# Performance work log

Measured on AMD Instinct MI355X. Metric: run time of the kernel, lower is better.

Reference implementation:

```python
import jax, jax.numpy as jnp
import numpy as np

HOP = 256
FRAMELEN = 512
FILTERLEN = 64
WD = FILTERLEN // 2          # weights_delay default
WMIN, WMAX = -65535.0, 65535.0
MU = 0.05                    # LMS step size (concrete iterate)
B = 2
NFRAMES = 4096
T = FRAMELEN + HOP * (NFRAMES - 1)


def _unfold(a, size, step):
    # torch.Tensor.unfold along last dim -> (..., n_frames, size)
    n = (a.shape[-1] - size) // step + 1
    idx = np.arange(n)[:, None] * step + np.arange(size)[None, :]
    return a[..., idx]


def setup_inputs() -> dict:
    key = jax.random.key(0)
    kd, kx = jax.random.split(key)
    d = jax.random.normal(kd, (B, T), dtype=jnp.float32)
    x = jax.random.normal(kx, (T,), dtype=jnp.float32)
    return {"d": d, "x": x}


def reference(d, x):
    d_f = _unfold(d, FRAMELEN, HOP)            # (B, F, framelen)
    x_f = _unfold(x, FRAMELEN, HOP)[None]      # (1, F, framelen)
    Bn, F, _ = d_f.shape
    S = (FRAMELEN - FILTERLEN) - WD            # sequential steps per frame
    w0 = jnp.zeros((Bn, F, FILTERLEN), d.dtype)

    def step(w, t):
        # x window [t : t+filterlen]  (i = WD + t in the torch loop)
        xi = jax.lax.dynamic_slice_in_dim(x_f, t, FILTERLEN, axis=2)  # (1,F,K)
        d_est = jnp.sum(w * xi, axis=-1)       # einsum('ijk,pjk->ij', w, xi)
        e = d_f[..., WD + t] - d_est
        w = jnp.clip(w + MU * e[..., None] * xi, WMIN, WMAX)
        return w, (d_est, e)

    _, (d_est_s, e_s) = jax.lax.scan(step, w0, jnp.arange(S))

    def assemble(y):
        # (S,B,F) -> (B,F, framelen-filterlen), first WD slots stay zero
        y = jnp.moveaxis(y, 0, -1)
        return jnp.pad(y, ((0, 0), (0, 0), (WD, 0)))

    d_est = assemble(d_est_s)
    e = assemble(e_s)
    tail = FRAMELEN - HOP

    def ola(y):
        # first frame in full, then non-overlapping tail of each later frame
        return jnp.concatenate(
            [y[:, 0, :], y[:, 1:, tail:].reshape(y.shape[0], -1)], axis=-1)

    return ola(d_est), ola(e)
```

## Files before the change

kernel.cpp:

```cpp
#include <hip/hip_runtime.h>

#define HOP     256
#define WD      32
#define NFRM    4096
#define TLEN    1048832
#define LROW    786688
#define XSTR    484
#define DSTR    420
#define XQn     121
#define DQn     105
#define XTOT    (2*XSTR + 16)
#define GTOT    (4*DSTR + 8)

__device__ __forceinline__ float red16(float v) {
    v += __int_as_float(__builtin_amdgcn_update_dpp(0, __float_as_int(v), 0xB1,  0xF, 0xF, true));
    v += __int_as_float(__builtin_amdgcn_update_dpp(0, __float_as_int(v), 0x4E,  0xF, 0xF, true));
    v += __int_as_float(__builtin_amdgcn_update_dpp(0, __float_as_int(v), 0x141, 0xF, 0xF, true));
    v += __int_as_float(__builtin_amdgcn_update_dpp(0, __float_as_int(v), 0x140, 0xF, 0xF, true));
    return v;
}

#define CL(v) __builtin_amdgcn_fmed3f((v), -65535.0f, 65535.0f)

#define STEP1(Xa,Xb,Xc,Xd, GV, IND) do {                          \
    float p = w0 * (Xa);                                          \
    p = fmaf(w1, (Xb), p);                                        \
    p = fmaf(w2, (Xc), p);                                        \
    p = fmaf(w3, (Xd), p);                                        \
    float s  = red16(p);                                          \
    so = fmaf((IND), s, so);                                      \
    float gm = fmaf(-0.05f, s, (GV));                             \
    w0 = CL(fmaf(gm, (Xa), w0));                                  \
    w1 = CL(fmaf(gm, (Xb), w1));                                  \
    w2 = CL(fmaf(gm, (Xc), w2));                                  \
    w3 = CL(fmaf(gm, (Xd), w3));                                  \
} while (0)

#define GROUP4(QA, QB, GQ, Ia, Ib, Ic, Id) do {                   \
    STEP1(QA.x,QA.y,QA.z,QA.w, GQ.x, Ia);                         \
    STEP1(QA.y,QA.z,QA.w,QB.x, GQ.y, Ib);                         \
    STEP1(QA.z,QA.w,QB.x,QB.y, GQ.z, Ic);                         \
    STEP1(QA.w,QB.x,QB.y,QB.z, GQ.w, Id);                         \
} while (0)

__global__ void __launch_bounds__(64, 2)
lms_kernel(const float* __restrict__ dmat, const float* __restrict__ xvec,
           float* __restrict__ out)
{
    __shared__ __align__(16) float lx[XTOT];
    __shared__ __align__(16) float lg[GTOT];

    const int tid = threadIdx.x;
    const int f0  = blockIdx.x * 2;

    for (int i = tid; i < 242 + 420; i += 64) {
        if (i < 242) {
            int fr = (i >= XQn) ? 1 : 0;
            int k  = i - fr * XQn;
            ((float4*)lx)[i] =
                *(const float4*)(xvec + (size_t)(f0 + fr) * HOP + 4 * k);
        } else {
            int j   = i - 242;
            int idx = j / DQn, k = j - idx * DQn;
            int b = idx >> 1, r = idx & 1;
            float4 v = *(const float4*)(dmat + (size_t)b * TLEN
                                        + (size_t)(f0 + r) * HOP + WD + 4 * k);
            float4 g2;
            g2.x = 0.05f * v.x; g2.y = 0.05f * v.y;
            g2.z = 0.05f * v.z; g2.w = 0.05f * v.w;
            ((float4*)lg)[j] = g2;
        }
    }
    __syncthreads();

    const int lane = tid & 63;
    const int row  = lane >> 4;
    const int col  = lane & 15;
    const int fl   = row >> 1;
    const int b    = row & 1;
    const int f    = f0 + fl;
    const bool early = (f == 0);
    const int ci   = b * 2 + fl;

    const float4* __restrict__ xq  = (const float4*)(lx + fl * XSTR + 4 * col);
    const float4* __restrict__ gq  = (const float4*)(lg + ci * DSTR);
    const float*  __restrict__ lgs = lg + ci * DSTR;

    float* od = out + (size_t)b * LROW + 32 + (size_t)192 * f;
    float* oe = od + 2 * (size_t)LROW;

    if (blockIdx.x == 0) {
        int pos = tid & 31;
        for (int r2 = tid >> 5; r2 < 4; r2 += 2)
            out[(size_t)r2 * LROW + pos] = 0.0f;
    }

    const float i0  = (col ==  0) ? 1.f : 0.f, i1  = (col ==  1) ? 1.f : 0.f;
    const float i2  = (col ==  2) ? 1.f : 0.f, i3  = (col ==  3) ? 1.f : 0.f;
    const float i4  = (col ==  4) ? 1.f : 0.f, i5  = (col ==  5) ? 1.f : 0.f;
    const float i6  = (col ==  6) ? 1.f : 0.f, i7  = (col ==  7) ? 1.f : 0.f;
    const float i8  = (col ==  8) ? 1.f : 0.f, i9  = (col ==  9) ? 1.f : 0.f;
    const float i10 = (col == 10) ? 1.f : 0.f, i11 = (col == 11) ? 1.f : 0.f;
    const float i12 = (col == 12) ? 1.f : 0.f, i13 = (col == 13) ? 1.f : 0.f;
    const float i14 = (col == 14) ? 1.f : 0.f, i15 = (col == 15) ? 1.f : 0.f;

    float w0 = 0.f, w1 = 0.f, w2 = 0.f, w3 = 0.f;

    float4 X0 = xq[0], X1 = xq[1], X2 = xq[2];
    float4 G0 = gq[0], G1 = gq[1];

    for (int j = 0; j < 26; ++j) {
        const int g = 4 * j;
        float so  = 0.f;
        float gvs = lgs[16 * j + col];

        float4 X3 = xq[g+3];  float4 G2 = gq[g+2];
        GROUP4(X0, X1, G0, i0,  i1,  i2,  i3);

        X0 = xq[g+4];         float4 G3 = gq[g+3];
        GROUP4(X1, X2, G1, i4,  i5,  i6,  i7);

        X1 = xq[g+5];         G0 = gq[g+4];
        GROUP4(X2, X3, G2, i8,  i9,  i10, i11);

        X2 = xq[g+6];         G1 = gq[g+5];
        GROUP4(X3, X0, G3, i12, i13, i14, i15);

        if (j >= 14 || early) {
            float gms = fmaf(-0.05f, so, gvs);
            od[16 * j + col] = so;
            oe[16 * j + col] = 20.0f * gms;
        }
    }
}

extern "C" void kernel_launch(void* const* d_in, const int* in_sizes, int n_in,
                              void* d_out, int out_size, void* d_ws, size_t ws_size,
                              hipStream_t stream) {
    const float* dmat = (const float*)d_in[0];
    const float* xvec = (const float*)d_in[1];
    float* out = (float*)d_out;

    hipLaunchKernelGGL(lms_kernel, dim3(NFRM / 2), dim3(64), 0, stream,
                       dmat, xvec, out);
}
```

Baseline: 36.93 us.

## Interleave two independent LMS chains per lane to hide DPP reduction latency

Each wave now handles four frames instead of two, and each lane advances two independent frame recurrences (A and B) in lockstep. This interleaves their dot-product, DPP reduction and weight-update chains so one chain's latency can overlap the other's. The dot product is also split into two partial sums to shorten the dependency depth. The trade-off is half as many blocks (1024), more registers and LDS per block, and launch bounds lowered to one block per SIMD, which reduces wave-level parallelism across the GPU.

```diff
diff --git a/kernel.cpp b/kernel.cpp
--- a/kernel.cpp
+++ b/kernel.cpp
@@ -9,41 +9,47 @@
 #define DSTR    420
 #define XQn     121
 #define DQn     105
-#define XTOT    (2*XSTR + 16)
-#define GTOT    (4*DSTR + 8)
+#define XTOT    (4*XSTR + 16)
+#define GTOT    (8*DSTR + 8)
 
-__device__ __forceinline__ float red16(float v) {
-    v += __int_as_float(__builtin_amdgcn_update_dpp(0, __float_as_int(v), 0xB1,  0xF, 0xF, true));
-    v += __int_as_float(__builtin_amdgcn_update_dpp(0, __float_as_int(v), 0x4E,  0xF, 0xF, true));
-    v += __int_as_float(__builtin_amdgcn_update_dpp(0, __float_as_int(v), 0x141, 0xF, 0xF, true));
-    v += __int_as_float(__builtin_amdgcn_update_dpp(0, __float_as_int(v), 0x140, 0xF, 0xF, true));
-    return v;
+template<int C>
+__device__ __forceinline__ float dpa(float v) {
+    return v + __int_as_float(
+        __builtin_amdgcn_update_dpp(0, __float_as_int(v), C, 0xF, 0xF, true));
 }
 
 #define CL(v) __builtin_amdgcn_fmed3f((v), -65535.0f, 65535.0f)
 
-#define STEP1(Xa,Xb,Xc,Xd, GV, IND) do {                          \
-    float p = w0 * (Xa);                                          \
-    p = fmaf(w1, (Xb), p);                                        \
-    p = fmaf(w2, (Xc), p);                                        \
-    p = fmaf(w3, (Xd), p);                                        \
-    float s  = red16(p);                                          \
-    so = fmaf((IND), s, so);                                      \
-    float gm = fmaf(-0.05f, s, (GV));                             \
-    w0 = CL(fmaf(gm, (Xa), w0));                                  \
-    w1 = CL(fmaf(gm, (Xb), w1));                                  \
-    w2 = CL(fmaf(gm, (Xc), w2));                                  \
-    w3 = CL(fmaf(gm, (Xd), w3));                                  \
+#define STEP2(AXa,AXb,AXc,AXd,AGV, BXa,BXb,BXc,BXd,BGV, IND) do {        \
+    float ap0 = aw0 * (AXa);             float bp0 = bw0 * (BXa);        \
+    float ap1 = aw2 * (AXc);             float bp1 = bw2 * (BXc);        \
+    ap0 = fmaf(aw1, (AXb), ap0);         bp0 = fmaf(bw1, (BXb), bp0);    \
+    ap1 = fmaf(aw3, (AXd), ap1);         bp1 = fmaf(bw3, (BXd), bp1);    \
+    float ap = ap0 + ap1;                float bp = bp0 + bp1;           \
+    ap = dpa<0xB1>(ap);                  bp = dpa<0xB1>(bp);             \
+    ap = dpa<0x4E>(ap);                  bp = dpa<0x4E>(bp);             \
+    ap = dpa<0x141>(ap);                 bp = dpa<0x141>(bp);            \
+    ap = dpa<0x140>(ap);                 bp = dpa<0x140>(bp);            \
+    aso = fmaf((IND), ap, aso);          bso = fmaf((IND), bp, bso);     \
+    float agm = fmaf(-0.05f, ap, (AGV)); float bgm = fmaf(-0.05f, bp, (BGV)); \
+    aw0 = CL(fmaf(agm, (AXa), aw0));     bw0 = CL(fmaf(bgm, (BXa), bw0)); \
+    aw1 = CL(fmaf(agm, (AXb), aw1));     bw1 = CL(fmaf(bgm, (BXb), bw1)); \
+    aw2 = CL(fmaf(agm, (AXc), aw2));     bw2 = CL(fmaf(bgm, (BXc), bw2)); \
+    aw3 = CL(fmaf(agm, (AXd), aw3));     bw3 = CL(fmaf(bgm, (BXd), bw3)); \
 } while (0)
 
-#define GROUP4(QA, QB, GQ, Ia, Ib, Ic, Id) do {                   \
-    STEP1(QA.x,QA.y,QA.z,QA.w, GQ.x, Ia);                         \
-    STEP1(QA.y,QA.z,QA.w,QB.x, GQ.y, Ib);                         \
-    STEP1(QA.z,QA.w,QB.x,QB.y, GQ.z, Ic);                         \
-    STEP1(QA.w,QB.x,QB.y,QB.z, GQ.w, Id);                         \
+#define GROUP2(AQA,AQB,AGQ, BQA,BQB,BGQ, Ia,Ib,Ic,Id) do {               \
+    STEP2(AQA.x,AQA.y,AQA.z,AQA.w, AGQ.x,                                \
+          BQA.x,BQA.y,BQA.z,BQA.w, BGQ.x, Ia);                           \
+    STEP2(AQA.y,AQA.z,AQA.w,AQB.x, AGQ.y,                                \
+          BQA.y,BQA.z,BQA.w,BQB.x, BGQ.y, Ib);                           \
+    STEP2(AQA.z,AQA.w,AQB.x,AQB.y, AGQ.z,                                \
+          BQA.z,BQA.w,BQB.x,BQB.y, BGQ.z, Ic);                           \
+    STEP2(AQA.w,AQB.x,AQB.y,AQB.z, AGQ.w,                                \
+          BQA.w,BQB.x,BQB.y,BQB.z, BGQ.w, Id);                           \
 } while (0)
 
-__global__ void __launch_bounds__(64, 2)
+__global__ void __launch_bounds__(64, 1)
 lms_kernel(const float* __restrict__ dmat, const float* __restrict__ xvec,
            float* __restrict__ out)
 {
@@ -51,18 +57,17 @@
     __shared__ __align__(16) float lg[GTOT];
 
     const int tid = threadIdx.x;
-    const int f0  = blockIdx.x * 2;
+    const int f0  = blockIdx.x * 4;
 
-    for (int i = tid; i < 242 + 420; i += 64) {
-        if (i < 242) {
-            int fr = (i >= XQn) ? 1 : 0;
-            int k  = i - fr * XQn;
+    for (int i = tid; i < 484 + 840; i += 64) {
+        if (i < 484) {
+            int fr = i / XQn, k = i - fr * XQn;
             ((float4*)lx)[i] =
                 *(const float4*)(xvec + (size_t)(f0 + fr) * HOP + 4 * k);
         } else {
-            int j   = i - 242;
+            int j   = i - 484;
             int idx = j / DQn, k = j - idx * DQn;
-            int b = idx >> 1, r = idx & 1;
+            int b = idx >> 2, r = idx & 3;
             float4 v = *(const float4*)(dmat + (size_t)b * TLEN
                                         + (size_t)(f0 + r) * HOP + WD + 4 * k);
             float4 g2;
@@ -73,26 +78,31 @@
     }
     __syncthreads();
 
-    const int lane = tid & 63;
-    const int row  = lane >> 4;
-    const int col  = lane & 15;
-    const int fl   = row >> 1;
+    const int row  = tid >> 4;
+    const int col  = tid & 15;
+    const int flA  = row >> 1;
     const int b    = row & 1;
-    const int f    = f0 + fl;
-    const bool early = (f == 0);
-    const int ci   = b * 2 + fl;
+    const int fA   = f0 + flA;
+    const int fB   = fA + 2;
+    const bool earlyA = (fA == 0);
+    const int ciA  = b * 4 + flA;
+    const int ciB  = ciA + 2;
 
-    const float4* __restrict__ xq  = (const float4*)(lx + fl * XSTR + 4 * col);
-    const float4* __restrict__ gq  = (const float4*)(lg + ci * DSTR);
-    const float*  __restrict__ lgs = lg + ci * DSTR;
+    const float4* __restrict__ xqA = (const float4*)(lx + flA * XSTR + 4 * col);
+    const float4* __restrict__ xqB = (const float4*)(lx + (flA + 2) * XSTR + 4 * col);
+    const float4* __restrict__ gqA = (const float4*)(lg + ciA * DSTR);
+    const float4* __restrict__ gqB = (const float4*)(lg + ciB * DSTR);
+    const float*  __restrict__ lgsA = lg + ciA * DSTR;
+    const float*  __restrict__ lgsB = lg + ciB * DSTR;
 
-    float* od = out + (size_t)b * LROW + 32 + (size_t)192 * f;
-    float* oe = od + 2 * (size_t)LROW;
+    float* odA = out + (size_t)b * LROW + 32 + (size_t)192 * fA;
+    float* oeA = odA + 2 * (size_t)LROW;
+    float* odB = out + (size_t)b * LROW + 32 + (size_t)192 * fB;
+    float* oeB = odB + 2 * (size_t)LROW;
 
     if (blockIdx.x == 0) {
-        int pos = tid & 31;
-        for (int r2 = tid >> 5; r2 < 4; r2 += 2)
-            out[(size_t)r2 * LROW + pos] = 0.0f;
+        for (int z = tid; z < 128; z += 64)
+            out[(size_t)(z >> 5) * LROW + (z & 31)] = 0.0f;
     }
 
     const float i0  = (col ==  0) ? 1.f : 0.f, i1  = (col ==  1) ? 1.f : 0.f;
@@ -104,32 +114,45 @@
     const float i12 = (col == 12) ? 1.f : 0.f, i13 = (col == 13) ? 1.f : 0.f;
     const float i14 = (col == 14) ? 1.f : 0.f, i15 = (col == 15) ? 1.f : 0.f;
 
-    float w0 = 0.f, w1 = 0.f, w2 = 0.f, w3 = 0.f;
+    float aw0=0.f, aw1=0.f, aw2=0.f, aw3=0.f;
+    float bw0=0.f, bw1=0.f, bw2=0.f, bw3=0.f;
 
-    float4 X0 = xq[0], X1 = xq[1], X2 = xq[2];
-    float4 G0 = gq[0], G1 = gq[1];
+    float4 aX0 = xqA[0], aX1 = xqA[1], aX2 = xqA[2];
+    float4 bX0 = xqB[0], bX1 = xqB[1], bX2 = xqB[2];
+    float4 aG0 = gqA[0], aG1 = gqA[1];
+    float4 bG0 = gqB[0], bG1 = gqB[1];
 
     for (int j = 0; j < 26; ++j) {
         const int g = 4 * j;
-        float so  = 0.f;
-        float gvs = lgs[16 * j + col];
+        float aso = 0.f, bso = 0.f;
+        float agvs = lgsA[16 * j + col];
+        float bgvs = lgsB[16 * j + col];
 
-        float4 X3 = xq[g+3];  float4 G2 = gq[g+2];
-        GROUP4(X0, X1, G0, i0,  i1,  i2,  i3);
+        float4 aX3 = xqA[g+3];  float4 aG2 = gqA[g+2];
+        float4 bX3 = xqB[g+3];  float4 bG2 = gqB[g+2];
+        GROUP2(aX0, aX1, aG0,  bX0, bX1, bG0,  i0,  i1,  i2,  i3);
 
-        X0 = xq[g+4];         float4 G3 = gq[g+3];
-        GROUP4(X1, X2, G1, i4,  i5,  i6,  i7);
+        aX0 = xqA[g+4];         float4 aG3 = gqA[g+3];
+        bX0 = xqB[g+4];         float4 bG3 = gqB[g+3];
+        GROUP2(aX1, aX2, aG1,  bX1, bX2, bG1,  i4,  i5,  i6,  i7);
 
-        X1 = xq[g+5];         G0 = gq[g+4];
-        GROUP4(X2, X3, G2, i8,  i9,  i10, i11);
+        aX1 = xqA[g+5];         aG0 = gqA[g+4];
+        bX1 = xqB[g+5];         bG0 = gqB[g+4];
+        GROUP2(aX2, aX3, aG2,  bX2, bX3, bG2,  i8,  i9,  i10, i11);
 
-        X2 = xq[g+6];         G1 = gq[g+5];
-        GROUP4(X3, X0, G3, i12, i13, i14, i15);
+        aX2 = xqA[g+6];         aG1 = gqA[g+5];
+        bX2 = xqB[g+6];         bG1 = gqB[g+5];
+        GROUP2(aX3, aX0, aG3,  bX3, bX0, bG3,  i12, i13, i14, i15);
 
-        if (j >= 14 || early) {
-            float gms = fmaf(-0.05f, so, gvs);
-            od[16 * j + col] = so;
-            oe[16 * j + col] = 20.0f * gms;
+        if (j >= 14 || earlyA) {
+            float agms = fmaf(-0.05f, aso, agvs);
+            odA[16 * j + col] = aso;
+            oeA[16 * j + col] = 20.0f * agms;
+        }
+        if (j >= 14) {
+            float bgms = fmaf(-0.05f, bso, bgvs);
+            odB[16 * j + col] = bso;
+            oeB[16 * j + col] = 20.0f * bgms;
         }
     }
 }
@@ -141,6 +164,6 @@
     const float* xvec = (const float*)d_in[1];
     float* out = (float*)d_out;
 
-    hipLaunchKernelGGL(lms_kernel, dim3(NFRM / 2), dim3(64), 0, stream,
+    hipLaunchKernelGGL(lms_kernel, dim3(NFRM / 4), dim3(64), 0, stream,
                        dmat, xvec, out);
 }
```

Result: slower. 48.45 us (+31.2%).

## Map each LMS chain to 4 lanes with 16 taps each, 8 frames per block

Applied to the files above, without the earlier changes.

Each (frame, batch) LMS chain now runs on 4 lanes holding 16 filter taps each, where it used to run on 16 lanes holding 4 taps. The dot-product reduction therefore shrinks from a 4-stage to a 2-stage DPP butterfly, which shortens the serial per-step dependency chain. A block now covers 8 frames with 16 chains per wave, so the grid has a quarter as many blocks. In exchange each lane carries many more registers and does more serial FMA work per step, and a smaller grid with larger shared-memory staging may reduce latency hiding and occupancy.

```diff
diff --git a/kernel.cpp b/kernel.cpp
--- a/kernel.cpp
+++ b/kernel.cpp
@@ -5,42 +5,56 @@
 #define NFRM    4096
 #define TLEN    1048832
 #define LROW    786688
+#define FPB     8
 #define XSTR    484
 #define DSTR    420
 #define XQn     121
 #define DQn     105
-#define XTOT    (2*XSTR + 16)
-#define GTOT    (4*DSTR + 8)
+#define XTOT    (FPB*XSTR + 16)
+#define GTOT    (16*DSTR + 16)
 
-__device__ __forceinline__ float red16(float v) {
-    v += __int_as_float(__builtin_amdgcn_update_dpp(0, __float_as_int(v), 0xB1,  0xF, 0xF, true));
-    v += __int_as_float(__builtin_amdgcn_update_dpp(0, __float_as_int(v), 0x4E,  0xF, 0xF, true));
-    v += __int_as_float(__builtin_amdgcn_update_dpp(0, __float_as_int(v), 0x141, 0xF, 0xF, true));
-    v += __int_as_float(__builtin_amdgcn_update_dpp(0, __float_as_int(v), 0x140, 0xF, 0xF, true));
+__device__ __forceinline__ float red4(float v) {
+    v += __int_as_float(__builtin_amdgcn_update_dpp(0, __float_as_int(v), 0xB1, 0xF, 0xF, true));
+    v += __int_as_float(__builtin_amdgcn_update_dpp(0, __float_as_int(v), 0x4E, 0xF, 0xF, true));
     return v;
 }
 
 #define CL(v) __builtin_amdgcn_fmed3f((v), -65535.0f, 65535.0f)
 
-#define STEP1(Xa,Xb,Xc,Xd, GV, IND) do {                          \
-    float p = w0 * (Xa);                                          \
-    p = fmaf(w1, (Xb), p);                                        \
-    p = fmaf(w2, (Xc), p);                                        \
-    p = fmaf(w3, (Xd), p);                                        \
-    float s  = red16(p);                                          \
-    so = fmaf((IND), s, so);                                      \
-    float gm = fmaf(-0.05f, s, (GV));                             \
-    w0 = CL(fmaf(gm, (Xa), w0));                                  \
-    w1 = CL(fmaf(gm, (Xb), w1));                                  \
-    w2 = CL(fmaf(gm, (Xc), w2));                                  \
-    w3 = CL(fmaf(gm, (Xd), w3));                                  \
+#define STEPX(GV, IND, SO, EO, \
+    X0,X1,X2,X3,X4,X5,X6,X7,X8,X9,Xa,Xb,Xc,Xd,Xe,Xf) do {            \
+    float pA = w0*(X0);  pA = fmaf(w1,(X1),pA);                       \
+    pA = fmaf(w2,(X2),pA);  pA = fmaf(w3,(X3),pA);                    \
+    float pB = w4*(X4);  pB = fmaf(w5,(X5),pB);                       \
+    pB = fmaf(w6,(X6),pB);  pB = fmaf(w7,(X7),pB);                    \
+    float pC = w8*(X8);  pC = fmaf(w9,(X9),pC);                       \
+    pC = fmaf(wa,(Xa),pC);  pC = fmaf(wb,(Xb),pC);                    \
+    float pD = wc*(Xc);  pD = fmaf(wd,(Xd),pD);                       \
+    pD = fmaf(we,(Xe),pD);  pD = fmaf(wf,(Xf),pD);                    \
+    float p  = (pA + pB) + (pC + pD);                                 \
+    float s  = red4(p);                                               \
+    SO = fmaf((IND), s, SO);                                          \
+    float gm = fmaf(-0.05f, s, (GV));                                 \
+    EO = fmaf((IND), gm, EO);                                         \
+    w0 = CL(fmaf(gm,(X0),w0));  w1 = CL(fmaf(gm,(X1),w1));            \
+    w2 = CL(fmaf(gm,(X2),w2));  w3 = CL(fmaf(gm,(X3),w3));            \
+    w4 = CL(fmaf(gm,(X4),w4));  w5 = CL(fmaf(gm,(X5),w5));            \
+    w6 = CL(fmaf(gm,(X6),w6));  w7 = CL(fmaf(gm,(X7),w7));            \
+    w8 = CL(fmaf(gm,(X8),w8));  w9 = CL(fmaf(gm,(X9),w9));            \
+    wa = CL(fmaf(gm,(Xa),wa));  wb = CL(fmaf(gm,(Xb),wb));            \
+    wc = CL(fmaf(gm,(Xc),wc));  wd = CL(fmaf(gm,(Xd),wd));            \
+    we = CL(fmaf(gm,(Xe),we));  wf = CL(fmaf(gm,(Xf),wf));            \
 } while (0)
 
-#define GROUP4(QA, QB, GQ, Ia, Ib, Ic, Id) do {                   \
-    STEP1(QA.x,QA.y,QA.z,QA.w, GQ.x, Ia);                         \
-    STEP1(QA.y,QA.z,QA.w,QB.x, GQ.y, Ib);                         \
-    STEP1(QA.z,QA.w,QB.x,QB.y, GQ.z, Ic);                         \
-    STEP1(QA.w,QB.x,QB.y,QB.z, GQ.w, Id);                         \
+#define PHASE(Q0,Q1,Q2,Q3,Q4, G4, SO, EO) do {                        \
+    STEPX(G4.x, i0, SO, EO, Q0.x,Q0.y,Q0.z,Q0.w, Q1.x,Q1.y,Q1.z,Q1.w,\
+          Q2.x,Q2.y,Q2.z,Q2.w, Q3.x,Q3.y,Q3.z,Q3.w);                  \
+    STEPX(G4.y, i1, SO, EO, Q0.y,Q0.z,Q0.w,Q1.x, Q1.y,Q1.z,Q1.w,Q2.x,\
+          Q2.y,Q2.z,Q2.w,Q3.x, Q3.y,Q3.z,Q3.w,Q4.x);                  \
+    STEPX(G4.z, i2, SO, EO, Q0.z,Q0.w,Q1.x,Q1.y, Q1.z,Q1.w,Q2.x,Q2.y,\
+          Q2.z,Q2.w,Q3.x,Q3.y, Q3.z,Q3.w,Q4.x,Q4.y);                  \
+    STEPX(G4.w, i3, SO, EO, Q0.w,Q1.x,Q1.y,Q1.z, Q1.w,Q2.x,Q2.y,Q2.z,\
+          Q2.w,Q3.x,Q3.y,Q3.z, Q3.w,Q4.x,Q4.y,Q4.z);                  \
 } while (0)
 
 __global__ void __launch_bounds__(64, 2)
@@ -51,40 +65,36 @@
     __shared__ __align__(16) float lg[GTOT];
 
     const int tid = threadIdx.x;
-    const int f0  = blockIdx.x * 2;
+    const int f0  = blockIdx.x * FPB;
 
-    for (int i = tid; i < 242 + 420; i += 64) {
-        if (i < 242) {
-            int fr = (i >= XQn) ? 1 : 0;
-            int k  = i - fr * XQn;
-            ((float4*)lx)[i] =
+    for (int i = tid; i < 968 + 1680; i += 64) {
+        if (i < 968) {
+            int fr = i / XQn, k = i - fr * XQn;
+            ((float4*)lx)[fr * XQn + k] =
                 *(const float4*)(xvec + (size_t)(f0 + fr) * HOP + 4 * k);
         } else {
-            int j   = i - 242;
-            int idx = j / DQn, k = j - idx * DQn;
-            int b = idx >> 1, r = idx & 1;
+            int j2 = i - 968;
+            int ch = j2 / DQn, k = j2 - ch * DQn;
+            int b = ch & 1, r = ch >> 1;
             float4 v = *(const float4*)(dmat + (size_t)b * TLEN
                                         + (size_t)(f0 + r) * HOP + WD + 4 * k);
             float4 g2;
             g2.x = 0.05f * v.x; g2.y = 0.05f * v.y;
             g2.z = 0.05f * v.z; g2.w = 0.05f * v.w;
-            ((float4*)lg)[j] = g2;
+            ((float4*)lg)[ch * DQn + k] = g2;
         }
     }
     __syncthreads();
 
-    const int lane = tid & 63;
-    const int row  = lane >> 4;
-    const int col  = lane & 15;
-    const int fl   = row >> 1;
-    const int b    = row & 1;
-    const int f    = f0 + fl;
+    const int ch = tid >> 2;
+    const int c  = tid & 3;
+    const int fl = ch >> 1;
+    const int b  = ch & 1;
+    const int f  = f0 + fl;
     const bool early = (f == 0);
-    const int ci   = b * 2 + fl;
 
-    const float4* __restrict__ xq  = (const float4*)(lx + fl * XSTR + 4 * col);
-    const float4* __restrict__ gq  = (const float4*)(lg + ci * DSTR);
-    const float*  __restrict__ lgs = lg + ci * DSTR;
+    const float4* __restrict__ xq = (const float4*)(lx + fl * XSTR + 16 * c);
+    const float4* __restrict__ gq = (const float4*)(lg + ch * DSTR);
 
     float* od = out + (size_t)b * LROW + 32 + (size_t)192 * f;
     float* oe = od + 2 * (size_t)LROW;
@@ -95,42 +105,39 @@
             out[(size_t)r2 * LROW + pos] = 0.0f;
     }
 
-    const float i0  = (col ==  0) ? 1.f : 0.f, i1  = (col ==  1) ? 1.f : 0.f;
-    const float i2  = (col ==  2) ? 1.f : 0.f, i3  = (col ==  3) ? 1.f : 0.f;
-    const float i4  = (col ==  4) ? 1.f : 0.f, i5  = (col ==  5) ? 1.f : 0.f;
-    const float i6  = (col ==  6) ? 1.f : 0.f, i7  = (col ==  7) ? 1.f : 0.f;
-    const float i8  = (col ==  8) ? 1.f : 0.f, i9  = (col ==  9) ? 1.f : 0.f;
-    const float i10 = (col == 10) ? 1.f : 0.f, i11 = (col == 11) ? 1.f : 0.f;
-    const float i12 = (col == 12) ? 1.f : 0.f, i13 = (col == 13) ? 1.f : 0.f;
-    const float i14 = (col == 14) ? 1.f : 0.f, i15 = (col == 15) ? 1.f : 0.f;
+    const float i0 = (c == 0) ? 1.f : 0.f, i1 = (c == 1) ? 1.f : 0.f;
+    const float i2 = (c == 2) ? 1.f : 0.f, i3 = (c == 3) ? 1.f : 0.f;
 
-    float w0 = 0.f, w1 = 0.f, w2 = 0.f, w3 = 0.f;
+    float w0=0.f,w1=0.f,w2=0.f,w3=0.f,w4=0.f,w5=0.f,w6=0.f,w7=0.f,
+          w8=0.f,w9=0.f,wa=0.f,wb=0.f,wc=0.f,wd=0.f,we=0.f,wf=0.f;
 
-    float4 X0 = xq[0], X1 = xq[1], X2 = xq[2];
-    float4 G0 = gq[0], G1 = gq[1];
+    float4 W0 = xq[0], W1 = xq[1], W2 = xq[2], W3 = xq[3],
+           W4 = xq[4], W5 = xq[5], W6 = xq[6], W7 = xq[7];
 
+    #pragma unroll 1
     for (int j = 0; j < 26; ++j) {
-        const int g = 4 * j;
-        float so  = 0.f;
-        float gvs = lgs[16 * j + col];
+        float4 Ga = gq[4*j],   Gb = gq[4*j+1],
+               Gc = gq[4*j+2], Gd = gq[4*j+3];
+        float4 N0 = xq[4*j+8],  N1 = xq[4*j+9],
+               N2 = xq[4*j+10], N3 = xq[4*j+11];
 
-        float4 X3 = xq[g+3];  float4 G2 = gq[g+2];
-        GROUP4(X0, X1, G0, i0,  i1,  i2,  i3);
+        float so0=0.f,so1=0.f,so2=0.f,so3=0.f;
+        float eo0=0.f,eo1=0.f,eo2=0.f,eo3=0.f;
 
-        X0 = xq[g+4];         float4 G3 = gq[g+3];
-        GROUP4(X1, X2, G1, i4,  i5,  i6,  i7);
-
-        X1 = xq[g+5];         G0 = gq[g+4];
-        GROUP4(X2, X3, G2, i8,  i9,  i10, i11);
-
-        X2 = xq[g+6];         G1 = gq[g+5];
-        GROUP4(X3, X0, G3, i12, i13, i14, i15);
+        PHASE(W0,W1,W2,W3,W4, Ga, so0, eo0);
+        PHASE(W1,W2,W3,W4,W5, Gb, so1, eo1);
+        PHASE(W2,W3,W4,W5,W6, Gc, so2, eo2);
+        PHASE(W3,W4,W5,W6,W7, Gd, so3, eo3);
 
         if (j >= 14 || early) {
-            float gms = fmaf(-0.05f, so, gvs);
-            od[16 * j + col] = so;
-            oe[16 * j + col] = 20.0f * gms;
+            od[16*j +  0 + c] = so0;  oe[16*j +  0 + c] = 20.0f * eo0;
+            od[16*j +  4 + c] = so1;  oe[16*j +  4 + c] = 20.0f * eo1;
+            od[16*j +  8 + c] = so2;  oe[16*j +  8 + c] = 20.0f * eo2;
+            od[16*j + 12 + c] = so3;  oe[16*j + 12 + c] = 20.0f * eo3;
         }
+
+        W0 = W4; W1 = W5; W2 = W6; W3 = W7;
+        W4 = N0; W5 = N1; W6 = N2; W7 = N3;
     }
 }
 
@@ -141,6 +148,6 @@
     const float* xvec = (const float*)d_in[1];
     float* out = (float*)d_out;
 
-    hipLaunchKernelGGL(lms_kernel, dim3(NFRM / 2), dim3(64), 0, stream,
+    hipLaunchKernelGGL(lms_kernel, dim3(NFRM / FPB), dim3(64), 0, stream,
                        dmat, xvec, out);
 }
```

Result: slower. 59.73 us (+61.7%).
